# Kernel optimization log

Hardware: AMD Instinct MI355X
Metric: run time of the kernel (lower is better)

## Reference

```python
import jax, jax.numpy as jnp
import numpy as np

B, N, CIN, DIM = 4, 16384, 32, 256
NPOINT, NNEIGH = 2048, 16
BN_EPS = 1e-5


def setup_inputs() -> dict:
    key = jax.random.key(0)
    ks = jax.random.split(key, 6)
    return {
        "xyz": jax.random.normal(ks[0], (B, N, 3), jnp.float32),
        "points": jax.random.normal(ks[1], (B, N, CIN), jnp.float32),
        "fc1_w": jax.random.normal(ks[2], (CIN, DIM), jnp.float32) * 0.05,
        "fc1_b": jnp.zeros((DIM,), jnp.float32),
        "conv1_w": jax.random.normal(ks[3], (DIM, DIM), jnp.float32) * 0.05,
        "conv1_b": jnp.zeros((DIM,), jnp.float32),
        "conv2_w": jax.random.normal(ks[4], (DIM, DIM), jnp.float32) * 0.05,
        "conv2_b": jnp.zeros((DIM,), jnp.float32),
        "bn1_g": jnp.ones((DIM,), jnp.float32),
        "bn1_b": jnp.zeros((DIM,), jnp.float32),
        "bn2_g": jnp.ones((DIM,), jnp.float32),
        "bn2_b": jnp.zeros((DIM,), jnp.float32),
        "bn_g": jnp.ones((DIM,), jnp.float32),
        "bn_b": jnp.zeros((DIM,), jnp.float32),
        "npoint": NPOINT,
        "nneigh": NNEIGH,
    }


def _gather(p, i):
    # p: [B, N, ...], i: [B, ...int] -> per-batch fancy index
    return jax.vmap(lambda a, b: a[b])(p, i)


def _batchnorm(x, g, b):
    # x: [B, S, C]; torch BatchNorm1d training-mode forward over (B, S)
    m = x.mean((0, 1), keepdims=True)
    v = x.var((0, 1), keepdims=True)  # biased variance, as torch uses in forward
    return (x - m) * jax.lax.rsqrt(v + BN_EPS) * g + b


def _fps(xyz, npoint):
    # furthest point sampling, seeded at index 0 (pointnet2_utils convention)
    Bn, Nn, _ = xyz.shape
    dist0 = jnp.full((Bn, Nn), jnp.inf, xyz.dtype)
    far0 = jnp.zeros((Bn,), jnp.int32)

    def step(carry, _):
        dist, far = carry
        cent = _gather(xyz, far)  # [B, 3]
        d = jnp.sum((xyz - cent[:, None, :]) ** 2, axis=-1)  # [B, N]
        dist = jnp.minimum(dist, d)
        nxt = jnp.argmax(dist, axis=-1).astype(jnp.int32)
        return (dist, nxt), far

    _, idx = jax.lax.scan(step, (dist0, far0), None, length=npoint)
    return idx.T  # [B, npoint]


def _square_distance(a, b):
    # a: [B, S, 3], b: [B, N, 3] -> [B, S, N]
    return (jnp.sum(a * a, -1)[..., :, None]
            + jnp.sum(b * b, -1)[..., None, :]
            - 2.0 * jnp.einsum('bsc,bnc->bsn', a, b))


def reference(xyz, points, fc1_w, fc1_b, conv1_w, conv1_b, conv2_w, conv2_b,
              bn1_g, bn1_b, bn2_g, bn2_b, bn_g, bn_b, npoint, nneigh):
    fps_idx = _fps(jax.lax.stop_gradient(xyz), npoint)          # [B, S]
    new_xyz = _gather(xyz, fps_idx)                              # [B, S, 3]

    h = points @ fc1_w + fc1_b                                   # [B, N, D]
    points_ori = _gather(h, fps_idx)                             # [B, S, D]

    t = jax.nn.relu(_batchnorm(h @ conv1_w.T + conv1_b, bn1_g, bn1_b))
    h = h + jax.nn.relu(_batchnorm(t @ conv2_w.T + conv2_b, bn2_g, bn2_b))

    d = _square_distance(jax.lax.stop_gradient(new_xyz), jax.lax.stop_gradient(xyz))
    _, idx = jax.lax.top_k(-d, nneigh)                           # [B, S, K] smallest dists
    grouped = _gather(h, idx)                                    # [B, S, K, D]
    new_points = points_ori + grouped.max(axis=2)                # [B, S, D]
    new_points = _batchnorm(new_points, bn_g, bn_b)
    return new_xyz, new_points
```

## Files before the change

### kernel.cpp

```cpp
#include <hip/hip_runtime.h>
#include <math.h>

#define Bn   4
#define Nn   16384
#define CINn 32
#define DIMn 256
#define Sn   2048
#define KNEI 16
#define BNEPS 1e-5f
#define MROWS (Bn * Nn)
#define SROWS (Bn * Sn)

#define NWORK 248
#define NBLK  (NWORK + Bn)

struct FusedSync {
    unsigned stage[8];
    unsigned prog[Bn];
};

#define UMAX_DPP(v, ctl, rmask)                                               \
    {                                                                         \
        unsigned _o = (unsigned)__builtin_amdgcn_update_dpp(                  \
            0, (int)(v), (ctl), (rmask), 0xf, true);                          \
        (v) = ((v) > _o) ? (v) : _o;                                          \
    }
#define WAVE_UMAX64(v)                                                        \
    UMAX_DPP(v, 0x111, 0xf) UMAX_DPP(v, 0x112, 0xf) UMAX_DPP(v, 0x114, 0xf)  \
    UMAX_DPP(v, 0x118, 0xf) UMAX_DPP(v, 0x142, 0xa) UMAX_DPP(v, 0x143, 0xc)
#define U64MAX_DPP16(khi, klo, ctl)                                           \
    {                                                                         \
        unsigned _lo2 = (unsigned)__builtin_amdgcn_update_dpp(                \
            0, (int)(klo), (ctl), 0xf, 0xf, true);                            \
        unsigned _hi2 = (unsigned)__builtin_amdgcn_update_dpp(                \
            0, (int)(khi), (ctl), 0xf, 0xf, true);                            \
        const bool _g = (_hi2 > (khi)) || (_hi2 == (khi) && _lo2 > (klo));    \
        (khi) = _g ? _hi2 : (khi);                                            \
        (klo) = _g ? _lo2 : (klo);                                            \
    }

__global__ __launch_bounds__(64) void fps_zero_kernel(unsigned* __restrict__ s)
{
    if (threadIdx.x < 12) s[threadIdx.x] = 0u;
}

template <bool BT, bool AFF>
__device__ void gemm_team(const float* A, const float* Bm, const float* bias,
                          const float* asc, const float* ash, float* C,
                          int K, int tile, bool act, float* lAs, float* lBs,
                          int ts)
{
    const int tx = ts & 15;
    const int ty = ts >> 4;
    const int r0 = (tile >> 2) * 64;
    const int c0 = (tile & 3) * 64;
    const int rrA = ts >> 2;
    const int kkA = (ts & 3) * 4;
    float acc[4][4] = {};
    for (int kc = 0; kc < K; kc += 16) {
        if (act) {
            const float4 v = *reinterpret_cast<const float4*>(
                &A[(size_t)(r0 + rrA) * K + kc + kkA]);
            const float vv[4] = {v.x, v.y, v.z, v.w};
#pragma unroll
            for (int m = 0; m < 4; ++m) {
                float xv = vv[m];
                if (AFF) {
                    const int k = kc + kkA + m;
                    xv = fmaxf(fmaf(xv, asc[k], ash[k]), 0.0f);
                }
                lAs[(kkA + m) * 64 + rrA] = xv;
            }
            if (BT) {
                const float4 u = *reinterpret_cast<const float4*>(
                    &Bm[(size_t)(c0 + rrA) * K + kc + kkA]);
                lBs[(kkA + 0) * 64 + rrA] = u.x;
                lBs[(kkA + 1) * 64 + rrA] = u.y;
                lBs[(kkA + 2) * 64 + rrA] = u.z;
                lBs[(kkA + 3) * 64 + rrA] = u.w;
            } else {
                const int kk = ts >> 4;
                const int cc = (ts & 15) * 4;
                const float4 u = *reinterpret_cast<const float4*>(
                    &Bm[(size_t)(kc + kk) * DIMn + c0 + cc]);
                *reinterpret_cast<float4*>(&lBs[kk * 64 + cc]) = u;
            }
        }
        __syncthreads();
        if (act) {
#pragma unroll
            for (int kk = 0; kk < 16; ++kk) {
                const float4 a = *reinterpret_cast<const float4*>(&lAs[kk * 64 + ty * 4]);
                const float4 bv = *reinterpret_cast<const float4*>(&lBs[kk * 64 + tx * 4]);
                const float av[4] = {a.x, a.y, a.z, a.w};
                const float bw[4] = {bv.x, bv.y, bv.z, bv.w};
#pragma unroll
                for (int i = 0; i < 4; ++i)
#pragma unroll
                    for (int j = 0; j < 4; ++j)
                        acc[i][j] = fmaf(av[i], bw[j], acc[i][j]);
            }
        }
        __syncthreads();
    }
    if (act) {
        const int c = c0 + tx * 4;
#pragma unroll
        for (int i = 0; i < 4; ++i) {
            float4 o;
            o.x = acc[i][0] + bias[c + 0];
            o.y = acc[i][1] + bias[c + 1];
            o.z = acc[i][2] + bias[c + 2];
            o.w = acc[i][3] + bias[c + 3];
            *reinterpret_cast<float4*>(&C[(size_t)(r0 + ty * 4 + i) * DIMn + c]) = o;
        }
    }
}

__device__ inline void stage_sync(unsigned* ctr, int t)
{
    __syncthreads();
    if (t == 0) {
        __hip_atomic_fetch_add(ctr, 1u, __ATOMIC_RELEASE, __HIP_MEMORY_SCOPE_AGENT);
        while (__hip_atomic_load(ctr, __ATOMIC_ACQUIRE, __HIP_MEMORY_SCOPE_AGENT)
               < (unsigned)NWORK)
            __builtin_amdgcn_s_sleep(2);
    }
    __syncthreads();
}

__global__ __launch_bounds__(1024, 1) void fused_kernel(
    const float* __restrict__ xyz, const float* __restrict__ points,
    const float* __restrict__ fc1_w, const float* __restrict__ fc1_b,
    const float* __restrict__ conv1_w, const float* __restrict__ conv1_b,
    const float* __restrict__ conv2_w, const float* __restrict__ conv2_b,
    const float* __restrict__ bn1_g, const float* __restrict__ bn1_b,
    const float* __restrict__ bn2_g, const float* __restrict__ bn2_b,
    float* __restrict__ h0, float* __restrict__ A1, float* __restrict__ A2,
    float* __restrict__ pre, int* __restrict__ fidx,
    float* __restrict__ ps, float* __restrict__ pq, float* __restrict__ scv,
    float* __restrict__ newxyz, FusedSync* sync)
{
    __shared__ __align__(16) char smem[131072];
    __shared__ unsigned long long s_aux[33];
    __shared__ int s_nidx[KNEI];
    const int t = threadIdx.x;

    if (blockIdx.x < Bn) {
#pragma clang fp contract(off)
        float2* s_xy = reinterpret_cast<float2*>(smem);
        unsigned long long (*s_wk)[16] =
            reinterpret_cast<unsigned long long (*)[16]>(s_aux);
        const int b = blockIdx.x;
        const int w = t >> 6;
        const int lane = t & 63;
        const float* __restrict__ px = xyz + (size_t)b * Nn * 3;
        float z[16], dist[16];
#pragma unroll
        for (int jp = 0; jp < 8; ++jp) {
            const int u = jp * 1024 + t;
            const float x0 = px[6 * u + 0];
            const float y0 = px[6 * u + 1];
            z[2 * jp + 0]  = px[6 * u + 2];
            const float x1 = px[6 * u + 3];
            const float y1 = px[6 * u + 4];
            z[2 * jp + 1]  = px[6 * u + 5];
            float4 q; q.x = x0; q.y = y0; q.z = x1; q.w = y1;
            *reinterpret_cast<float4*>(&s_xy[2 * u]) = q;
            dist[2 * jp + 0] = __builtin_huge_valf();
            dist[2 * jp + 1] = __builtin_huge_valf();
        }
#pragma unroll
        for (int s = 0; s < 16; ++s) asm volatile("" : "+v"(z[s]));
        float cx = px[0], cy = px[1], cz = px[2];
        if (t == 0) {
            fidx[b * Sn] = 0;
            newxyz[(size_t)b * Sn * 3 + 0] = cx;
            newxyz[(size_t)b * Sn * 3 + 1] = cy;
            newxyz[(size_t)b * Sn * 3 + 2] = cz;
        }
        __syncthreads();
        for (int i = 0; i < Sn - 1; ++i) {
            float bd = -1.0f;
#pragma unroll
            for (int jp = 0; jp < 8; ++jp) {
                const float4 q =
                    *reinterpret_cast<const float4*>(&s_xy[2 * (jp * 1024 + t)]);
                {
                    const float dx = q.x - cx;
                    const float dy = q.y - cy;
                    const float dz = z[2 * jp] - cz;
                    const float d = (dx * dx + dy * dy) + dz * dz;
                    const float nd = fminf(dist[2 * jp], d);
                    dist[2 * jp] = nd;
                    bd = fmaxf(bd, nd);
                }
                {
                    const float dx = q.z - cx;
                    const float dy = q.w - cy;
                    const float dz = z[2 * jp + 1] - cz;
                    const float d = (dx * dx + dy * dy) + dz * dz;
                    const float nd = fminf(dist[2 * jp + 1], d);
                    dist[2 * jp + 1] = nd;
                    bd = fmaxf(bd, nd);
                }
            }
            unsigned bn = 0;
#pragma unroll
            for (int s = 15; s >= 0; --s)
                if (dist[s] == bd)
                    bn = 0xFFFFFFFFu -
                         (unsigned)(2 * ((s >> 1) * 1024 + t) + (s & 1));
            unsigned bdu = __float_as_uint(bd);
            unsigned m = bdu;
            WAVE_UMAX64(m)
            const unsigned bdw = (unsigned)__builtin_amdgcn_readlane((int)m, 63);
            unsigned q2 = (bdu == bdw) ? bn : 0u;
            WAVE_UMAX64(q2)
            const unsigned bnw = (unsigned)__builtin_amdgcn_readlane((int)q2, 63);
            if (lane == 0)
                s_wk[i & 1][w] = ((unsigned long long)bdw << 32) | bnw;
            __syncthreads();
            const unsigned long long kk = (lane < 16) ? s_wk[i & 1][lane] : 0ull;
            unsigned klo = (unsigned)kk;
            unsigned khi = (unsigned)(kk >> 32);
            U64MAX_DPP16(khi, klo, 0x111)
            U64MAX_DPP16(khi, klo, 0x112)
            U64MAX_DPP16(khi, klo, 0x114)
            U64MAX_DPP16(khi, klo, 0x118)
            const unsigned bnf = (unsigned)__builtin_amdgcn_readlane((int)klo, 15);
            const int wu = (int)(0xFFFFFFFFu - bnf);
            const float2 cxy = s_xy[wu];
            cx = cxy.x;
            cy = cxy.y;
            cz = px[3 * wu + 2];
            if (t == 0) {
                fidx[b * Sn + i + 1] = wu;
                newxyz[(size_t)(b * Sn + i + 1) * 3 + 0] = cx;
                newxyz[(size_t)(b * Sn + i + 1) * 3 + 1] = cy;
                newxyz[(size_t)(b * Sn + i + 1) * 3 + 2] = cz;
                if (((i + 2) & 255) == 0)
                    __hip_atomic_store(&sync->prog[b], (unsigned)(i + 2),
                                       __ATOMIC_RELEASE, __HIP_MEMORY_SCOPE_AGENT);
            }
        }
        return;
    }

    const int wid = blockIdx.x - Bn;
    const int team = t >> 8;
    const int ts = t & 255;
    float* lAs = reinterpret_cast<float*>(smem) + team * 2048;
    float* lBs = lAs + 1024;
    float* sc1 = scv, *sh1 = scv + 256, *sc2 = scv + 512, *sh2 = scv + 768;

    for (int it = 0; it < 5; ++it) {
        const int tile = it * (NWORK * 4) + wid * 4 + team;
        gemm_team<false, false>(points, fc1_w, fc1_b, nullptr, nullptr, h0,
                                CINn, tile, tile < 4096, lAs, lBs, ts);
    }
    stage_sync(&sync->stage[0], t);
    for (int it = 0; it < 5; ++it) {
        const int tile = it * (NWORK * 4) + wid * 4 + team;
        gemm_team<true, false>(h0, conv1_w, conv1_b, nullptr, nullptr, A1,
                               DIMn, tile, tile < 4096, lAs, lBs, ts);
    }
    stage_sync(&sync->stage[1], t);
    for (int sb = wid; sb < 256; sb += NWORK) {
        if (t < DIMn) {
            float s = 0.0f, q = 0.0f;
            const size_t r0 = (size_t)sb * 256;
            for (int r = 0; r < 256; ++r) {
                const float v = A1[(r0 + r) * DIMn + t];
                s += v;
                q = fmaf(v, v, q);
            }
            ps[sb * DIMn + t] = s;
            pq[sb * DIMn + t] = q;
        }
    }
    stage_sync(&sync->stage[2], t);
    if (wid == 0 && t < DIMn) {
        float s = 0.0f, q = 0.0f;
        for (int i = 0; i < 256; ++i) { s += ps[i * DIMn + t]; q += pq[i * DIMn + t]; }
        const float invN = 1.0f / MROWS;
        const float mean = s * invN;
        const float var = q * invN - mean * mean;
        const float r = 1.0f / sqrtf(var + BNEPS);
        const float scale = bn1_g[t] * r;
        sc1[t] = scale;
        sh1[t] = bn1_b[t] - mean * scale;
    }
    stage_sync(&sync->stage[3], t);
    for (int it = 0; it < 5; ++it) {
        const int tile = it * (NWORK * 4) + wid * 4 + team;
        gemm_team<true, true>(A1, conv2_w, conv2_b, sc1, sh1, A2,
                              DIMn, tile, tile < 4096, lAs, lBs, ts);
    }
    stage_sync(&sync->stage[4], t);
    for (int sb = wid; sb < 256; sb += NWORK) {
        if (t < DIMn) {
            float s = 0.0f, q = 0.0f;
            const size_t r0 = (size_t)sb * 256;
            for (int r = 0; r < 256; ++r) {
                const float v = A2[(r0 + r) * DIMn + t];
                s += v;
                q = fmaf(v, v, q);
            }
            ps[sb * DIMn + t] = s;
            pq[sb * DIMn + t] = q;
        }
    }
    stage_sync(&sync->stage[5], t);
    if (wid == 0 && t < DIMn) {
        float s = 0.0f, q = 0.0f;
        for (int i = 0; i < 256; ++i) { s += ps[i * DIMn + t]; q += pq[i * DIMn + t]; }
        const float invN = 1.0f / MROWS;
        const float mean = s * invN;
        const float var = q * invN - mean * mean;
        const float r = 1.0f / sqrtf(var + BNEPS);
        const float scale = bn2_g[t] * r;
        sc2[t] = scale;
        sh2[t] = bn2_b[t] - mean * scale;
    }
    stage_sync(&sync->stage[6], t);
    for (size_t idx = (size_t)wid * 1024 + t; idx < (size_t)MROWS * DIMn / 4;
         idx += (size_t)NWORK * 1024) {
        const int c4 = (int)(idx & 63);
        const float4 hv = reinterpret_cast<const float4*>(h0)[idx];
        float4 av = reinterpret_cast<float4*>(A2)[idx];
        const float4 s4 = reinterpret_cast<const float4*>(sc2)[c4];
        const float4 b4 = reinterpret_cast<const float4*>(sh2)[c4];
        av.x = hv.x + fmaxf(fmaf(av.x, s4.x, b4.x), 0.0f);
        av.y = hv.y + fmaxf(fmaf(av.y, s4.y, b4.y), 0.0f);
        av.z = hv.z + fmaxf(fmaf(av.z, s4.z, b4.z), 0.0f);
        av.w = hv.w + fmaxf(fmaf(av.w, s4.w, b4.w), 0.0f);
        reinterpret_cast<float4*>(A2)[idx] = av;
    }
    stage_sync(&sync->stage[7], t);

    {
#pragma clang fp contract(off)
        unsigned* s_key = reinterpret_cast<unsigned*>(smem);
        const int b = wid & 3;
        const int w = t >> 6;
        const int lane = t & 63;
        const float* px = xyz + (size_t)b * Nn * 3;
        unsigned cprog = 0;
        for (int q = wid; q < SROWS; q += NWORK) {
            const int s = q >> 2;
            if (t == 0 && cprog < (unsigned)(s + 1)) {
                unsigned p;
                do {
                    p = __hip_atomic_load(&sync->prog[b], __ATOMIC_ACQUIRE,
                                          __HIP_MEMORY_SCOPE_AGENT);
                    if (p < (unsigned)(s + 1)) __builtin_amdgcn_s_sleep(8);
                } while (p < (unsigned)(s + 1));
                cprog = p;
            }
            __syncthreads();
            const int bs = b * Sn + s;
            const float qx = newxyz[(size_t)bs * 3 + 0];
            const float qy = newxyz[(size_t)bs * 3 + 1];
            const float qz = newxyz[(size_t)bs * 3 + 2];
            const float qq = (qx * qx + qy * qy) + qz * qz;
            unsigned long long mkey = ~0ull;
#pragma unroll 4
            for (int u = 0; u < 16; ++u) {
                const int n = t + (u << 10);
                const float bx = px[n * 3 + 0];
                const float by = px[n * 3 + 1];
                const float bz = px[n * 3 + 2];
                const float bb2 = (bx * bx + by * by) + bz * bz;
                const float ab = (qx * bx + qy * by) + qz * bz;
                const float d = (qq + bb2) - 2.0f * ab;
                unsigned u32 = __float_as_uint(d);
                u32 = ((int)u32 < 0) ? ~u32 : (u32 | 0x80000000u);
                s_key[n] = u32;
                const unsigned long long k =
                    ((unsigned long long)u32 << 32) | (unsigned)n;
                mkey = (k < mkey) ? k : mkey;
            }
            __syncthreads();
            for (int r = 0; r < KNEI; ++r) {
                unsigned long long k = mkey;
#pragma unroll
                for (int off = 32; off > 0; off >>= 1) {
                    const unsigned long long o = __shfl_xor(k, off);
                    k = (o < k) ? o : k;
                }
                if (lane == 0) s_aux[w] = k;
                __syncthreads();
                if (w == 0) {
                    unsigned long long kk = (lane < 16) ? s_aux[lane] : ~0ull;
#pragma unroll
                    for (int off = 8; off > 0; off >>= 1) {
                        const unsigned long long o = __shfl_xor(kk, off);
                        kk = (o < kk) ? o : kk;
                    }
                    if (lane == 0) {
                        s_aux[32] = kk;
                        s_nidx[r] = (int)(unsigned)(kk & 0xFFFFFFFFull);
                    }
                }
                __syncthreads();
                const unsigned long long wk = s_aux[32];
                if (wk == mkey) {
                    const int wn = (int)(unsigned)(wk & 0xFFFFFFFFull);
                    s_key[wn] = 0xFFFFFFFFu;
                    mkey = ~0ull;
#pragma unroll 4
                    for (int u = 0; u < 16; ++u) {
                        const int n = t + (u << 10);
                        const unsigned long long kk2 =
                            ((unsigned long long)s_key[n] << 32) | (unsigned)n;
                        mkey = (kk2 < mkey) ? kk2 : mkey;
                    }
                }
            }
            __syncthreads();
            if (t < DIMn) {
                const int fid = fidx[bs];
                const float po = h0[((size_t)b * Nn + fid) * DIMn + t];
                float m = -__builtin_huge_valf();
#pragma unroll
                for (int r = 0; r < KNEI; ++r) {
                    const int n = s_nidx[r];
                    m = fmaxf(m, A2[((size_t)b * Nn + n) * DIMn + t]);
                }
                pre[(size_t)bs * DIMn + t] = po + m;
            }
            __syncthreads();
        }
    }
}

__global__ __launch_bounds__(256) void stats_partial(const float* __restrict__ X,
                                                     int rowsPerBlk,
                                                     float* __restrict__ ps,
                                                     float* __restrict__ pq)
{
    const int c = threadIdx.x;
    const size_t r0 = (size_t)blockIdx.x * rowsPerBlk;
    float s = 0.0f, q = 0.0f;
    for (int r = 0; r < rowsPerBlk; ++r) {
        const float v = X[(r0 + r) * DIMn + c];
        s += v;
        q = fmaf(v, v, q);
    }
    ps[blockIdx.x * DIMn + c] = s;
    pq[blockIdx.x * DIMn + c] = q;
}

__global__ __launch_bounds__(256) void bn_finalize(const float* __restrict__ ps,
                                                   const float* __restrict__ pq,
                                                   int nblk, float invN,
                                                   const float* __restrict__ g,
                                                   const float* __restrict__ bb,
                                                   float* __restrict__ sc,
                                                   float* __restrict__ sh)
{
    const int c = threadIdx.x;
    float s = 0.0f, q = 0.0f;
    for (int i = 0; i < nblk; ++i) {
        s += ps[i * DIMn + c];
        q += pq[i * DIMn + c];
    }
    const float mean = s * invN;
    const float var = q * invN - mean * mean;
    const float r = 1.0f / sqrtf(var + BNEPS);
    const float scale = g[c] * r;
    sc[c] = scale;
    sh[c] = bb[c] - mean * scale;
}

__global__ __launch_bounds__(256) void apply_bn_kernel(const float* __restrict__ pre,
                                                       const float* __restrict__ sc,
                                                       const float* __restrict__ sh,
                                                       float* __restrict__ out)
{
    const size_t i = (size_t)blockIdx.x * 256 + threadIdx.x;
    const int c4 = (int)(i & 63);
    const float4 v = reinterpret_cast<const float4*>(pre)[i];
    const float4 s4 = reinterpret_cast<const float4*>(sc)[c4];
    const float4 b4 = reinterpret_cast<const float4*>(sh)[c4];
    float4 o;
    o.x = fmaf(v.x, s4.x, b4.x);
    o.y = fmaf(v.y, s4.y, b4.y);
    o.z = fmaf(v.z, s4.z, b4.z);
    o.w = fmaf(v.w, s4.w, b4.w);
    reinterpret_cast<float4*>(out)[i] = o;
}

extern "C" void kernel_launch(void* const* d_in, const int* in_sizes, int n_in,
                              void* d_out, int out_size, void* d_ws, size_t ws_size,
                              hipStream_t stream)
{
    (void)in_sizes; (void)n_in; (void)out_size; (void)ws_size;
    const float* xyz     = (const float*)d_in[0];
    const float* points  = (const float*)d_in[1];
    const float* fc1_w   = (const float*)d_in[2];
    const float* fc1_b   = (const float*)d_in[3];
    const float* conv1_w = (const float*)d_in[4];
    const float* conv1_b = (const float*)d_in[5];
    const float* conv2_w = (const float*)d_in[6];
    const float* conv2_b = (const float*)d_in[7];
    const float* bn1_g   = (const float*)d_in[8];
    const float* bn1_b   = (const float*)d_in[9];
    const float* bn2_g   = (const float*)d_in[10];
    const float* bn2_b   = (const float*)d_in[11];
    const float* bn_g    = (const float*)d_in[12];
    const float* bn_b    = (const float*)d_in[13];

    float* out = (float*)d_out;
    float* newxyz = out;
    float* outpts = out + (size_t)Bn * Sn * 3;

    char* w = (char*)d_ws;
    float* h0   = (float*)(w);
    float* A1   = (float*)(w + (64ull << 20));
    float* A2   = (float*)(w + (128ull << 20));
    float* pre  = (float*)(w + (192ull << 20));
    int*   fidx = (int*)  (w + (200ull << 20));
    float* ps   = (float*)(w + (201ull << 20));
    float* pq   = ps + 256 * 256;
    float* scv  = pq + 256 * 256;
    float* sc3  = scv + 1024;
    float* sh3  = sc3 + 256;
    FusedSync* sync = (FusedSync*)(w + (203ull << 20));

    fps_zero_kernel<<<1, 64, 0, stream>>>((unsigned*)sync);
    fused_kernel<<<NBLK, 1024, 0, stream>>>(
        xyz, points, fc1_w, fc1_b, conv1_w, conv1_b, conv2_w, conv2_b,
        bn1_g, bn1_b, bn2_g, bn2_b, h0, A1, A2, pre, fidx, ps, pq, scv,
        newxyz, sync);
    stats_partial<<<64, 256, 0, stream>>>(pre, SROWS / 64, ps, pq);
    bn_finalize<<<1, 256, 0, stream>>>(ps, pq, 64, 1.0f / SROWS, bn_g, bn_b, sc3, sh3);
    apply_bn_kernel<<<(SROWS * DIMn / 4) / 256, 256, 0, stream>>>(pre, sc3, sh3, outpts);
}
```

Before: 4.120 ms.

## Pack FPS xyz layout, forward winner z via LDS, batch index writes

Reworks the furthest-point-sampling loop. Coordinates are repacked into float4 {x0,x1,y0,y1}, and distance math uses 2-wide vector types so the compiler can emit packed FP32 ops. The winning point's z is sent through shared memory per wave instead of being reloaded from global memory on the serial critical path. The fidx/newxyz writes are buffered in LDS and flushed every 256 iterations before the progress release. This adds ballot/shuffle work and extra barriers at each flush.

```diff
diff --git a/kernel.cpp b/kernel.cpp
--- a/kernel.cpp
+++ b/kernel.cpp
@@ -13,6 +13,8 @@
 
 #define NWORK 248
 #define NBLK  (NWORK + Bn)
+
+typedef float f32x2 __attribute__((ext_vector_type(2)));
 
 struct FusedSync {
     unsigned stage[8];
@@ -143,83 +145,77 @@
 {
     __shared__ __align__(16) char smem[131072];
     __shared__ unsigned long long s_aux[33];
+    __shared__ float s_wz[2][16];
+    __shared__ __align__(16) float4 s_obuf[256];
     __shared__ int s_nidx[KNEI];
     const int t = threadIdx.x;
 
     if (blockIdx.x < Bn) {
 #pragma clang fp contract(off)
-        float2* s_xy = reinterpret_cast<float2*>(smem);
+        float4* s_xy4 = reinterpret_cast<float4*>(smem);
         unsigned long long (*s_wk)[16] =
             reinterpret_cast<unsigned long long (*)[16]>(s_aux);
         const int b = blockIdx.x;
         const int w = t >> 6;
         const int lane = t & 63;
         const float* __restrict__ px = xyz + (size_t)b * Nn * 3;
-        float z[16], dist[16];
+        f32x2 z2[8], dist2[8];
 #pragma unroll
         for (int jp = 0; jp < 8; ++jp) {
             const int u = jp * 1024 + t;
-            const float x0 = px[6 * u + 0];
-            const float y0 = px[6 * u + 1];
-            z[2 * jp + 0]  = px[6 * u + 2];
-            const float x1 = px[6 * u + 3];
-            const float y1 = px[6 * u + 4];
-            z[2 * jp + 1]  = px[6 * u + 5];
-            float4 q; q.x = x0; q.y = y0; q.z = x1; q.w = y1;
-            *reinterpret_cast<float4*>(&s_xy[2 * u]) = q;
-            dist[2 * jp + 0] = __builtin_huge_valf();
-            dist[2 * jp + 1] = __builtin_huge_valf();
-        }
-#pragma unroll
-        for (int s = 0; s < 16; ++s) asm volatile("" : "+v"(z[s]));
+            const float2 q0 = *reinterpret_cast<const float2*>(&px[6 * u + 0]);
+            const float2 q1 = *reinterpret_cast<const float2*>(&px[6 * u + 2]);
+            const float2 q2 = *reinterpret_cast<const float2*>(&px[6 * u + 4]);
+            float4 pk; pk.x = q0.x; pk.y = q1.y; pk.z = q0.y; pk.w = q2.x;
+            s_xy4[u] = pk;
+            z2[jp] = f32x2{q1.x, q2.y};
+            dist2[jp] = f32x2{__builtin_huge_valf(), __builtin_huge_valf()};
+        }
+#pragma unroll
+        for (int p = 0; p < 8; ++p) asm volatile("" : "+v"(z2[p]));
         float cx = px[0], cy = px[1], cz = px[2];
         if (t == 0) {
-            fidx[b * Sn] = 0;
-            newxyz[(size_t)b * Sn * 3 + 0] = cx;
-            newxyz[(size_t)b * Sn * 3 + 1] = cy;
-            newxyz[(size_t)b * Sn * 3 + 2] = cz;
+            float4 o0; o0.x = cx; o0.y = cy; o0.z = cz; o0.w = __int_as_float(0);
+            s_obuf[0] = o0;
         }
         __syncthreads();
         for (int i = 0; i < Sn - 1; ++i) {
+            const f32x2 cx2 = {cx, cx}, cy2 = {cy, cy}, cz2 = {cz, cz};
             float bd = -1.0f;
 #pragma unroll
             for (int jp = 0; jp < 8; ++jp) {
-                const float4 q =
-                    *reinterpret_cast<const float4*>(&s_xy[2 * (jp * 1024 + t)]);
-                {
-                    const float dx = q.x - cx;
-                    const float dy = q.y - cy;
-                    const float dz = z[2 * jp] - cz;
-                    const float d = (dx * dx + dy * dy) + dz * dz;
-                    const float nd = fminf(dist[2 * jp], d);
-                    dist[2 * jp] = nd;
-                    bd = fmaxf(bd, nd);
-                }
-                {
-                    const float dx = q.z - cx;
-                    const float dy = q.w - cy;
-                    const float dz = z[2 * jp + 1] - cz;
-                    const float d = (dx * dx + dy * dy) + dz * dz;
-                    const float nd = fminf(dist[2 * jp + 1], d);
-                    dist[2 * jp + 1] = nd;
-                    bd = fmaxf(bd, nd);
-                }
+                const float4 q = s_xy4[jp * 1024 + t];
+                const f32x2 dx = f32x2{q.x, q.y} - cx2;
+                const f32x2 dy = f32x2{q.z, q.w} - cy2;
+                const f32x2 dz = z2[jp] - cz2;
+                const f32x2 dd = (dx * dx + dy * dy) + dz * dz;
+                const float n0 = fminf(dist2[jp].x, dd.x);
+                const float n1 = fminf(dist2[jp].y, dd.y);
+                dist2[jp] = f32x2{n0, n1};
+                bd = fmaxf(bd, fmaxf(n0, n1));
             }
             unsigned bn = 0;
-#pragma unroll
-            for (int s = 15; s >= 0; --s)
-                if (dist[s] == bd)
-                    bn = 0xFFFFFFFFu -
-                         (unsigned)(2 * ((s >> 1) * 1024 + t) + (s & 1));
-            unsigned bdu = __float_as_uint(bd);
+            float zb = 0.0f;
+#pragma unroll
+            for (int jp = 7; jp >= 0; --jp) {
+                const unsigned n0 = 2u * (unsigned)(jp * 1024 + t);
+                if (dist2[jp].y == bd) { bn = 0xFFFFFFFFu - (n0 + 1); zb = z2[jp].y; }
+                if (dist2[jp].x == bd) { bn = 0xFFFFFFFFu - n0;       zb = z2[jp].x; }
+            }
+            const unsigned bdu = __float_as_uint(bd);
             unsigned m = bdu;
             WAVE_UMAX64(m)
             const unsigned bdw = (unsigned)__builtin_amdgcn_readlane((int)m, 63);
             unsigned q2 = (bdu == bdw) ? bn : 0u;
             WAVE_UMAX64(q2)
             const unsigned bnw = (unsigned)__builtin_amdgcn_readlane((int)q2, 63);
-            if (lane == 0)
+            const unsigned long long wmask = __ballot(bdu == bdw && bn == bnw);
+            const int wl = __ffsll((unsigned long long)wmask) - 1;
+            const float zw = __shfl(zb, wl);
+            if (lane == 0) {
                 s_wk[i & 1][w] = ((unsigned long long)bdw << 32) | bnw;
+                s_wz[i & 1][w] = zw;
+            }
             __syncthreads();
             const unsigned long long kk = (lane < 16) ? s_wk[i & 1][lane] : 0ull;
             unsigned klo = (unsigned)kk;
@@ -230,16 +226,30 @@
             U64MAX_DPP16(khi, klo, 0x118)
             const unsigned bnf = (unsigned)__builtin_amdgcn_readlane((int)klo, 15);
             const int wu = (int)(0xFFFFFFFFu - bnf);
-            const float2 cxy = s_xy[wu];
-            cx = cxy.x;
-            cy = cxy.y;
-            cz = px[3 * wu + 2];
+            const int up = wu >> 1;
+            const int ww = (up & 1023) >> 6;
+            const float4 qw = s_xy4[up];
+            cx = (wu & 1) ? qw.y : qw.x;
+            cy = (wu & 1) ? qw.w : qw.z;
+            cz = s_wz[i & 1][ww];
             if (t == 0) {
-                fidx[b * Sn + i + 1] = wu;
-                newxyz[(size_t)(b * Sn + i + 1) * 3 + 0] = cx;
-                newxyz[(size_t)(b * Sn + i + 1) * 3 + 1] = cy;
-                newxyz[(size_t)(b * Sn + i + 1) * 3 + 2] = cz;
-                if (((i + 2) & 255) == 0)
+                float4 ob; ob.x = cx; ob.y = cy; ob.z = cz;
+                ob.w = __int_as_float(wu);
+                s_obuf[(i + 1) & 255] = ob;
+            }
+            if (((i + 2) & 255) == 0) {
+                __syncthreads();
+                const int cb = (i + 1) - 255;
+                if (t < 256) {
+                    const float4 v = s_obuf[t];
+                    const int bs = b * Sn + cb + t;
+                    newxyz[(size_t)bs * 3 + 0] = v.x;
+                    newxyz[(size_t)bs * 3 + 1] = v.y;
+                    newxyz[(size_t)bs * 3 + 2] = v.z;
+                    fidx[bs] = __float_as_int(v.w);
+                }
+                __syncthreads();
+                if (t == 0)
                     __hip_atomic_store(&sync->prog[b], (unsigned)(i + 2),
                                        __ATOMIC_RELEASE, __HIP_MEMORY_SCOPE_AGENT);
             }
```

New measurement: 3.825 ms. -7.1%, faster.
